# Optimization experiments

Measured on AMD Instinct MI355X. Metric: run time of the kernel, lower is better.

## Reference

```python
import jax, jax.numpy as jnp
import numpy as np

N = 100000
E = 1600000


def graph_conv(x, src, dst, W_rel, b_rel, W_root, n_nodes):
    # PyG GraphConv (aggr='add'): out = lin_rel(sum_j x_j) + lin_root(x)
    agg = jax.ops.segment_sum(x[src], dst, num_segments=n_nodes)  # [N, in]
    return agg @ W_rel + b_rel + x @ W_root


def _glorot(key, shape):
    fan_in = shape[0]
    return jax.random.normal(key, shape, dtype=jnp.float32) / jnp.sqrt(jnp.float32(fan_in))


def setup_inputs() -> dict:
    key = jax.random.key(0)
    ks = jax.random.split(key, 16)
    x = jax.random.normal(ks[0], (N, 48), dtype=jnp.float32)
    additional_x = jax.random.normal(ks[1], (N, 16), dtype=jnp.float32)
    lf_embedding = jax.random.normal(ks[2], (N, 16), dtype=jnp.float32)
    edge_index = jax.random.randint(ks[3], (2, E), 0, N, dtype=jnp.int64)
    # conv1: 64 -> 32 ; conv2: 48 -> 48 ; conv3: 48 -> 16
    return {
        "x": x,
        "edge_index": edge_index,
        "additional_x": additional_x,
        "lf_embedding": lf_embedding,
        "W1_rel": _glorot(ks[4], (64, 32)),
        "b1": jnp.zeros((32,), dtype=jnp.float32),
        "W1_root": _glorot(ks[5], (64, 32)),
        "W2_rel": _glorot(ks[6], (48, 48)),
        "b2": jnp.zeros((48,), dtype=jnp.float32),
        "W2_root": _glorot(ks[7], (48, 48)),
        "W3_rel": _glorot(ks[8], (48, 16)),
        "b3": jnp.zeros((16,), dtype=jnp.float32),
        "W3_root": _glorot(ks[9], (48, 16)),
    }


def reference(x, edge_index, additional_x, lf_embedding,
              W1_rel, b1, W1_root, W2_rel, b2, W2_root, W3_rel, b3, W3_root):
    src, dst = edge_index[0], edge_index[1]
    n = x.shape[0]
    h = jnp.concatenate([x, additional_x], axis=1)            # [N, 64]
    h = jax.nn.relu(graph_conv(h, src, dst, W1_rel, b1, W1_root, n))  # [N, 32]
    h = jnp.concatenate([h, lf_embedding], axis=1)            # [N, 48]
    h = jax.nn.relu(graph_conv(h, src, dst, W2_rel, b2, W2_root, n))  # [N, 48]
    h = graph_conv(h, src, dst, W3_rel, b3, W3_root, n)       # [N, 16]
    return h + additional_x
```

## Files before the change

kernel.cpp:

```cpp
#include <hip/hip_runtime.h>

#define NODES_MAX 100000
#define EDGES_MAX 1600000
#define BN 256
#define NBUCK ((NODES_MAX + BN - 1) / BN)
#define B_PART 256
#define SCAN_CHUNK 1024

__device__ float g_ws[(size_t)NODES_MAX * 160];
__device__ unsigned short g_tb[(size_t)NODES_MAX * 112];
__device__ int g_rowptr[NODES_MAX + 1];
__device__ int g_csr[EDGES_MAX];
__device__ unsigned g_be[EDGES_MAX];
__device__ int g_mat[NBUCK * B_PART];
__device__ int g_bsum[(NBUCK * B_PART + SCAN_CHUNK - 1) / SCAN_CHUNK + 1];

__device__ __forceinline__ unsigned short f2bf(float f) {
    union { float f; unsigned u; } c; c.f = f;
    unsigned r = (c.u + 0x7FFFu + ((c.u >> 16) & 1u)) >> 16;
    return (unsigned short)r;
}
__device__ __forceinline__ float bflo(unsigned u) {
    union { unsigned u; float f; } c; c.u = u << 16; return c.f;
}
__device__ __forceinline__ float bfhi(unsigned u) {
    union { unsigned u; float f; } c; c.u = u & 0xFFFF0000u; return c.f;
}

__global__ __launch_bounds__(1024) void k_bcount(const int* __restrict__ edge, int E,
                                                 int nbuck, int chunk) {
    __shared__ int h[NBUCK];
    for (int i = threadIdx.x; i < nbuck; i += 1024) h[i] = 0;
    __syncthreads();
    const int lo = blockIdx.x * chunk, hi = min(E, lo + chunk);
    for (int e = lo + threadIdx.x; e < hi; e += 1024)
        atomicAdd(&h[edge[E + e] >> 8], 1);
    __syncthreads();
    for (int k = threadIdx.x; k < nbuck; k += 1024)
        g_mat[k * B_PART + blockIdx.x] = h[k];
}

__global__ __launch_bounds__(256) void k_scan_local(int M) {
    __shared__ int ssum[256];
    const int tid = threadIdx.x;
    const int base = blockIdx.x * SCAN_CHUNK + tid * 4;
    int v0 = (base + 0 < M) ? g_mat[base + 0] : 0;
    int v1 = (base + 1 < M) ? g_mat[base + 1] : 0;
    int v2 = (base + 2 < M) ? g_mat[base + 2] : 0;
    int v3 = (base + 3 < M) ? g_mat[base + 3] : 0;
    int s = v0 + v1 + v2 + v3;
    ssum[tid] = s;
    __syncthreads();
    for (int off = 1; off < 256; off <<= 1) {
        int v = (tid >= off) ? ssum[tid - off] : 0;
        __syncthreads();
        ssum[tid] += v;
        __syncthreads();
    }
    int run = ssum[tid] - s;
    if (base + 0 < M) g_mat[base + 0] = run;
    run += v0;
    if (base + 1 < M) g_mat[base + 1] = run;
    run += v1;
    if (base + 2 < M) g_mat[base + 2] = run;
    run += v2;
    if (base + 3 < M) g_mat[base + 3] = run;
    if (tid == 255) g_bsum[blockIdx.x] = ssum[255];
}

__global__ __launch_bounds__(1024) void k_scan_bsums(int nb) {
    __shared__ int ssum[1024];
    const int tid = threadIdx.x;
    int s = (tid < nb) ? g_bsum[tid] : 0;
    ssum[tid] = s;
    __syncthreads();
    for (int off = 1; off < 1024; off <<= 1) {
        int v = (tid >= off) ? ssum[tid - off] : 0;
        __syncthreads();
        ssum[tid] += v;
        __syncthreads();
    }
    if (tid < nb) g_bsum[tid] = ssum[tid] - s;
}

__global__ __launch_bounds__(1024) void k_bpart(const int* __restrict__ edge, int E,
                                                int nbuck, int chunk) {
    __shared__ int cur[NBUCK];
    for (int k = threadIdx.x; k < nbuck; k += 1024) {
        int idx = k * B_PART + blockIdx.x;
        cur[k] = g_mat[idx] + g_bsum[idx >> 10];
    }
    __syncthreads();
    const int lo = blockIdx.x * chunk, hi = min(E, lo + chunk);
    for (int e = lo + threadIdx.x; e < hi; e += 1024) {
        int s = edge[e], d = edge[E + e];
        int pos = atomicAdd(&cur[d >> 8], 1);
        g_be[pos] = ((unsigned)s << 8) | (unsigned)(d & (BN - 1));
    }
}

__global__ __launch_bounds__(BN) void k_csr(int N, int E, int nbuck) {
    const int b = blockIdx.x;
    const int nlo = b * BN;
    const int ebase = g_mat[b * B_PART] + g_bsum[(b * B_PART) >> 10];
    const int eend = (b + 1 < nbuck)
        ? (g_mat[(b + 1) * B_PART] + g_bsum[((b + 1) * B_PART) >> 10]) : E;
    __shared__ int cnt[BN];
    __shared__ int pfx[BN];
    const int tid = threadIdx.x;
    cnt[tid] = 0;
    __syncthreads();
    for (int e = ebase + tid; e < eend; e += BN)
        atomicAdd(&cnt[g_be[e] & (BN - 1)], 1);
    __syncthreads();
    int v = cnt[tid];
    pfx[tid] = v;
    __syncthreads();
    for (int off = 1; off < BN; off <<= 1) {
        int t = (tid >= off) ? pfx[tid - off] : 0;
        __syncthreads();
        pfx[tid] += t;
        __syncthreads();
    }
    int excl = pfx[tid] - v;
    int n = nlo + tid;
    if (n < N) g_rowptr[n] = ebase + excl;
    if (b == 0 && tid == 0) g_rowptr[N] = E;
    cnt[tid] = excl;
    __syncthreads();
    for (int e = ebase + tid; e < eend; e += BN) {
        unsigned pv = g_be[e];
        int pos = atomicAdd(&cnt[pv & (BN - 1)], 1);
        g_csr[ebase + pos] = (int)(pv >> 8);
    }
}

template <int F, int RS>
__global__ __launch_bounds__(256) void k_gather_relu(size_t oTB, size_t oR, size_t oH, int N) {
    constexpr int L = F / 8;
    int tid = blockIdx.x * 256 + threadIdx.x;
    int node = tid / L, c = tid % L;
    if (node >= N) return;
    const unsigned short* __restrict__ tb = &g_tb[oTB];
    int j = g_rowptr[node];
    const int end = g_rowptr[node + 1];
    float s0 = 0.f, s1 = 0.f, s2 = 0.f, s3 = 0.f, s4 = 0.f, s5 = 0.f, s6 = 0.f, s7 = 0.f;
    for (; j + 3 < end; j += 4) {
        int sn0 = g_csr[j], sn1 = g_csr[j + 1], sn2 = g_csr[j + 2], sn3 = g_csr[j + 3];
        const uint4 v0 = *(const uint4*)&tb[(size_t)sn0 * RS + c * 8];
        const uint4 v1 = *(const uint4*)&tb[(size_t)sn1 * RS + c * 8];
        const uint4 v2 = *(const uint4*)&tb[(size_t)sn2 * RS + c * 8];
        const uint4 v3 = *(const uint4*)&tb[(size_t)sn3 * RS + c * 8];
        s0 += bflo(v0.x) + bflo(v1.x) + bflo(v2.x) + bflo(v3.x);
        s1 += bfhi(v0.x) + bfhi(v1.x) + bfhi(v2.x) + bfhi(v3.x);
        s2 += bflo(v0.y) + bflo(v1.y) + bflo(v2.y) + bflo(v3.y);
        s3 += bfhi(v0.y) + bfhi(v1.y) + bfhi(v2.y) + bfhi(v3.y);
        s4 += bflo(v0.z) + bflo(v1.z) + bflo(v2.z) + bflo(v3.z);
        s5 += bfhi(v0.z) + bfhi(v1.z) + bfhi(v2.z) + bfhi(v3.z);
        s6 += bflo(v0.w) + bflo(v1.w) + bflo(v2.w) + bflo(v3.w);
        s7 += bfhi(v0.w) + bfhi(v1.w) + bfhi(v2.w) + bfhi(v3.w);
    }
    for (; j < end; ++j) {
        int sn = g_csr[j];
        const uint4 v = *(const uint4*)&tb[(size_t)sn * RS + c * 8];
        s0 += bflo(v.x); s1 += bfhi(v.x);
        s2 += bflo(v.y); s3 += bfhi(v.y);
        s4 += bflo(v.z); s5 += bfhi(v.z);
        s6 += bflo(v.w); s7 += bfhi(v.w);
    }
    const size_t ro = oR + (size_t)node * F + c * 8;
    const float4 ra = *(const float4*)&g_ws[ro];
    const float4 rb = *(const float4*)&g_ws[ro + 4];
    float4 oa, ob;
    oa.x = fmaxf(s0 + ra.x, 0.f); oa.y = fmaxf(s1 + ra.y, 0.f);
    oa.z = fmaxf(s2 + ra.z, 0.f); oa.w = fmaxf(s3 + ra.w, 0.f);
    ob.x = fmaxf(s4 + rb.x, 0.f); ob.y = fmaxf(s5 + rb.y, 0.f);
    ob.z = fmaxf(s6 + rb.z, 0.f); ob.w = fmaxf(s7 + rb.w, 0.f);
    const size_t ho = oH + (size_t)node * F + c * 8;
    *(float4*)&g_ws[ho] = oa;
    *(float4*)&g_ws[ho + 4] = ob;
}

__global__ __launch_bounds__(256) void k_gather_out(size_t oTB, float* __restrict__ out, int N) {
    constexpr int F = 16, L = 2;
    int tid = blockIdx.x * 256 + threadIdx.x;
    int node = tid / L, c = tid % L;
    if (node >= N) return;
    const unsigned short* __restrict__ tb = &g_tb[oTB];
    int j = g_rowptr[node];
    const int end = g_rowptr[node + 1];
    float s0 = 0.f, s1 = 0.f, s2 = 0.f, s3 = 0.f, s4 = 0.f, s5 = 0.f, s6 = 0.f, s7 = 0.f;
    for (; j + 3 < end; j += 4) {
        int sn0 = g_csr[j], sn1 = g_csr[j + 1], sn2 = g_csr[j + 2], sn3 = g_csr[j + 3];
        const uint4 v0 = *(const uint4*)&tb[(size_t)sn0 * F + c * 8];
        const uint4 v1 = *(const uint4*)&tb[(size_t)sn1 * F + c * 8];
        const uint4 v2 = *(const uint4*)&tb[(size_t)sn2 * F + c * 8];
        const uint4 v3 = *(const uint4*)&tb[(size_t)sn3 * F + c * 8];
        s0 += bflo(v0.x) + bflo(v1.x) + bflo(v2.x) + bflo(v3.x);
        s1 += bfhi(v0.x) + bfhi(v1.x) + bfhi(v2.x) + bfhi(v3.x);
        s2 += bflo(v0.y) + bflo(v1.y) + bflo(v2.y) + bflo(v3.y);
        s3 += bfhi(v0.y) + bfhi(v1.y) + bfhi(v2.y) + bfhi(v3.y);
        s4 += bflo(v0.z) + bflo(v1.z) + bflo(v2.z) + bflo(v3.z);
        s5 += bfhi(v0.z) + bfhi(v1.z) + bfhi(v2.z) + bfhi(v3.z);
        s6 += bflo(v0.w) + bflo(v1.w) + bflo(v2.w) + bflo(v3.w);
        s7 += bfhi(v0.w) + bfhi(v1.w) + bfhi(v2.w) + bfhi(v3.w);
    }
    for (; j < end; ++j) {
        int sn = g_csr[j];
        const uint4 v = *(const uint4*)&tb[(size_t)sn * F + c * 8];
        s0 += bflo(v.x); s1 += bfhi(v.x);
        s2 += bflo(v.y); s3 += bfhi(v.y);
        s4 += bflo(v.z); s5 += bfhi(v.z);
        s6 += bflo(v.w); s7 += bfhi(v.w);
    }
    float* op = &out[(size_t)node * F + c * 8];
    float4 oa = *(float4*)op;
    float4 ob = *(float4*)(op + 4);
    oa.x += s0; oa.y += s1; oa.z += s2; oa.w += s3;
    ob.x += s4; ob.y += s5; ob.z += s6; ob.w += s7;
    *(float4*)op = oa;
    *(float4*)(op + 4) = ob;
}

#define L1_PADS 72
__global__ __launch_bounds__(512) void k_l1_transform(
        const float* __restrict__ x, const float* __restrict__ ax,
        const float* __restrict__ Wrel, const float* __restrict__ Wroot,
        const float* __restrict__ b, int N, size_t oTB1, size_t oR1) {
    __shared__ float sWrel[64 * 32];
    __shared__ float sWroot[64 * 32];
    __shared__ unsigned short sH[128 * L1_PADS];
    const int tid = threadIdx.x;
    if (tid < 512) {
        ((float4*)sWrel)[tid] = ((const float4*)Wrel)[tid];
        ((float4*)sWroot)[tid] = ((const float4*)Wroot)[tid];
    }
    const int n0 = blockIdx.x * 128;
    for (int i = tid; i < 128 * 16; i += 512) {
        int nl = i >> 4, g = i & 15, n = n0 + nl;
        float4 v = {0.f, 0.f, 0.f, 0.f};
        if (n < N) v = (g < 12) ? *(const float4*)&x[(size_t)n * 48 + g * 4]
                                : *(const float4*)&ax[(size_t)n * 16 + (g - 12) * 4];
        ushort4 hv;
        hv.x = f2bf(v.x); hv.y = f2bf(v.y); hv.z = f2bf(v.z); hv.w = f2bf(v.w);
        *(ushort4*)&sH[nl * L1_PADS + g * 4] = hv;
    }
    __syncthreads();
    const int jg = tid & 7, nlp = tid >> 3;
    const unsigned short* h0p = &sH[(nlp * 2 + 0) * L1_PADS];
    const unsigned short* h1p = &sH[(nlp * 2 + 1) * L1_PADS];
    float at[2][4] = {}, ar[2][4] = {};
    for (int k = 0; k < 64; ++k) {
        const float4 wr = *(const float4*)&sWrel[k * 32 + jg * 4];
        const float4 wo = *(const float4*)&sWroot[k * 32 + jg * 4];
        const float h0 = bflo(h0p[k]);
        const float h1 = bflo(h1p[k]);
        at[0][0] = fmaf(h0, wr.x, at[0][0]); at[0][1] = fmaf(h0, wr.y, at[0][1]);
        at[0][2] = fmaf(h0, wr.z, at[0][2]); at[0][3] = fmaf(h0, wr.w, at[0][3]);
        ar[0][0] = fmaf(h0, wo.x, ar[0][0]); ar[0][1] = fmaf(h0, wo.y, ar[0][1]);
        ar[0][2] = fmaf(h0, wo.z, ar[0][2]); ar[0][3] = fmaf(h0, wo.w, ar[0][3]);
        at[1][0] = fmaf(h1, wr.x, at[1][0]); at[1][1] = fmaf(h1, wr.y, at[1][1]);
        at[1][2] = fmaf(h1, wr.z, at[1][2]); at[1][3] = fmaf(h1, wr.w, at[1][3]);
        ar[1][0] = fmaf(h1, wo.x, ar[1][0]); ar[1][1] = fmaf(h1, wo.y, ar[1][1]);
        ar[1][2] = fmaf(h1, wo.z, ar[1][2]); ar[1][3] = fmaf(h1, wo.w, ar[1][3]);
    }
    const float4 bv = *(const float4*)&b[jg * 4];
    #pragma unroll
    for (int m = 0; m < 2; ++m) {
        int n = n0 + nlp * 2 + m;
        if (n < N) {
            ushort4 tv;
            tv.x = f2bf(at[m][0]); tv.y = f2bf(at[m][1]);
            tv.z = f2bf(at[m][2]); tv.w = f2bf(at[m][3]);
            *(ushort4*)&g_tb[oTB1 + (size_t)n * 32 + jg * 4] = tv;
            float4 rv;
            rv.x = ar[m][0] + bv.x; rv.y = ar[m][1] + bv.y;
            rv.z = ar[m][2] + bv.z; rv.w = ar[m][3] + bv.w;
            *(float4*)&g_ws[oR1 + (size_t)n * 32 + jg * 4] = rv;
        }
    }
}

#define L2_PAD 49
__global__ __launch_bounds__(384) void k_l2_transform(
        const float* __restrict__ lf,
        const float* __restrict__ Wrel, const float* __restrict__ Wroot,
        const float* __restrict__ b, int N,
        size_t oH1, size_t oTB2, size_t oR2) {
    __shared__ float sWrel[48 * 48];
    __shared__ float sWroot[48 * 48];
    __shared__ float sH[64 * L2_PAD];
    const int tid = threadIdx.x;
    for (int i = tid; i < 576; i += 384) {
        ((float4*)sWrel)[i] = ((const float4*)Wrel)[i];
        ((float4*)sWroot)[i] = ((const float4*)Wroot)[i];
    }
    const int n0 = blockIdx.x * 64;
    for (int i = tid; i < 64 * 48; i += 384) {
        int nl = i / 48, k = i % 48, n = n0 + nl;
        float v = 0.f;
        if (n < N) v = (k < 32) ? g_ws[oH1 + (size_t)n * 32 + k]
                                : lf[(size_t)n * 16 + (k - 32)];
        sH[nl * L2_PAD + k] = v;
    }
    __syncthreads();
    const int jg = tid % 12, nlp = tid / 12;
    const float* h0p = &sH[(nlp * 2 + 0) * L2_PAD];
    const float* h1p = &sH[(nlp * 2 + 1) * L2_PAD];
    float at[2][4] = {}, ar[2][4] = {};
    for (int k = 0; k < 48; ++k) {
        const float4 wr = *(const float4*)&sWrel[k * 48 + jg * 4];
        const float4 wo = *(const float4*)&sWroot[k * 48 + jg * 4];
        const float h0 = h0p[k];
        const float h1 = h1p[k];
        at[0][0] = fmaf(h0, wr.x, at[0][0]); at[0][1] = fmaf(h0, wr.y, at[0][1]);
        at[0][2] = fmaf(h0, wr.z, at[0][2]); at[0][3] = fmaf(h0, wr.w, at[0][3]);
        ar[0][0] = fmaf(h0, wo.x, ar[0][0]); ar[0][1] = fmaf(h0, wo.y, ar[0][1]);
        ar[0][2] = fmaf(h0, wo.z, ar[0][2]); ar[0][3] = fmaf(h0, wo.w, ar[0][3]);
        at[1][0] = fmaf(h1, wr.x, at[1][0]); at[1][1] = fmaf(h1, wr.y, at[1][1]);
        at[1][2] = fmaf(h1, wr.z, at[1][2]); at[1][3] = fmaf(h1, wr.w, at[1][3]);
        ar[1][0] = fmaf(h1, wo.x, ar[1][0]); ar[1][1] = fmaf(h1, wo.y, ar[1][1]);
        ar[1][2] = fmaf(h1, wo.z, ar[1][2]); ar[1][3] = fmaf(h1, wo.w, ar[1][3]);
    }
    const float4 bv = *(const float4*)&b[jg * 4];
    #pragma unroll
    for (int m = 0; m < 2; ++m) {
        int n = n0 + nlp * 2 + m;
        if (n < N) {
            ushort4 tv;
            tv.x = f2bf(at[m][0]); tv.y = f2bf(at[m][1]);
            tv.z = f2bf(at[m][2]); tv.w = f2bf(at[m][3]);
            *(ushort4*)&g_tb[oTB2 + (size_t)n * 64 + jg * 4] = tv;
            float4 rv;
            rv.x = ar[m][0] + bv.x; rv.y = ar[m][1] + bv.y;
            rv.z = ar[m][2] + bv.z; rv.w = ar[m][3] + bv.w;
            *(float4*)&g_ws[oR2 + (size_t)n * 48 + jg * 4] = rv;
        }
    }
}

#define L3_PAD 49
__global__ __launch_bounds__(256) void k_l3_transform(
        const float* __restrict__ ax,
        const float* __restrict__ Wrel, const float* __restrict__ Wroot,
        const float* __restrict__ b, int N,
        size_t oH2, size_t oTB3, float* __restrict__ out) {
    __shared__ float sWrel[48 * 16];
    __shared__ float sWroot[48 * 16];
    __shared__ float sH[128 * L3_PAD];
    const int tid = threadIdx.x;
    if (tid < 192) {
        ((float4*)sWrel)[tid] = ((const float4*)Wrel)[tid];
        ((float4*)sWroot)[tid] = ((const float4*)Wroot)[tid];
    }
    const int n0 = blockIdx.x * 128;
    for (int i = tid; i < 128 * 48; i += 256) {
        int nl = i / 48, k = i % 48, n = n0 + nl;
        sH[nl * L3_PAD + k] = (n < N) ? g_ws[oH2 + (size_t)n * 48 + k] : 0.f;
    }
    __syncthreads();
    const int jg = tid & 3, nlp = tid >> 2;
    const float* h0p = &sH[(nlp * 2 + 0) * L3_PAD];
    const float* h1p = &sH[(nlp * 2 + 1) * L3_PAD];
    float at[2][4] = {}, ar[2][4] = {};
    for (int k = 0; k < 48; ++k) {
        const float4 wr = *(const float4*)&sWrel[k * 16 + jg * 4];
        const float4 wo = *(const float4*)&sWroot[k * 16 + jg * 4];
        const float h0 = h0p[k];
        const float h1 = h1p[k];
        at[0][0] = fmaf(h0, wr.x, at[0][0]); at[0][1] = fmaf(h0, wr.y, at[0][1]);
        at[0][2] = fmaf(h0, wr.z, at[0][2]); at[0][3] = fmaf(h0, wr.w, at[0][3]);
        ar[0][0] = fmaf(h0, wo.x, ar[0][0]); ar[0][1] = fmaf(h0, wo.y, ar[0][1]);
        ar[0][2] = fmaf(h0, wo.z, ar[0][2]); ar[0][3] = fmaf(h0, wo.w, ar[0][3]);
        at[1][0] = fmaf(h1, wr.x, at[1][0]); at[1][1] = fmaf(h1, wr.y, at[1][1]);
        at[1][2] = fmaf(h1, wr.z, at[1][2]); at[1][3] = fmaf(h1, wr.w, at[1][3]);
        ar[1][0] = fmaf(h1, wo.x, ar[1][0]); ar[1][1] = fmaf(h1, wo.y, ar[1][1]);
        ar[1][2] = fmaf(h1, wo.z, ar[1][2]); ar[1][3] = fmaf(h1, wo.w, ar[1][3]);
    }
    const float4 bv = *(const float4*)&b[jg * 4];
    #pragma unroll
    for (int m = 0; m < 2; ++m) {
        int n = n0 + nlp * 2 + m;
        if (n < N) {
            ushort4 tv;
            tv.x = f2bf(at[m][0]); tv.y = f2bf(at[m][1]);
            tv.z = f2bf(at[m][2]); tv.w = f2bf(at[m][3]);
            *(ushort4*)&g_tb[oTB3 + (size_t)n * 16 + jg * 4] = tv;
            const float4 av = *(const float4*)&ax[(size_t)n * 16 + jg * 4];
            float4 rv;
            rv.x = ar[m][0] + bv.x + av.x; rv.y = ar[m][1] + bv.y + av.y;
            rv.z = ar[m][2] + bv.z + av.z; rv.w = ar[m][3] + bv.w + av.w;
            *(float4*)&out[(size_t)n * 16 + jg * 4] = rv;
        }
    }
}

extern "C" void kernel_launch(void* const* d_in, const int* in_sizes, int n_in,
                              void* d_out, int out_size, void* d_ws, size_t ws_size,
                              hipStream_t stream) {
    const float* x     = (const float*)d_in[0];
    const int*   edge  = (const int*)d_in[1];
    const float* ax    = (const float*)d_in[2];
    const float* lf    = (const float*)d_in[3];
    const float* W1rel = (const float*)d_in[4];
    const float* b1    = (const float*)d_in[5];
    const float* W1root= (const float*)d_in[6];
    const float* W2rel = (const float*)d_in[7];
    const float* b2    = (const float*)d_in[8];
    const float* W2root= (const float*)d_in[9];
    const float* W3rel = (const float*)d_in[10];
    const float* b3    = (const float*)d_in[11];
    const float* W3root= (const float*)d_in[12];
    float* out = (float*)d_out;

    const int N = in_sizes[0] / 48;
    const int E = in_sizes[1] / 2;
    const int nbuck = (N + BN - 1) / BN;
    const int chunk = (E + B_PART - 1) / B_PART;
    const int M = nbuck * B_PART;
    const int nb = (M + SCAN_CHUNK - 1) / SCAN_CHUNK;

    const size_t oR1 = 0;
    const size_t oH1 = (size_t)N * 32;
    const size_t oR2 = (size_t)N * 64;
    const size_t oH2 = (size_t)N * 112;
    const size_t oTB1 = 0;
    const size_t oTB2 = (size_t)N * 32;
    const size_t oTB3 = (size_t)N * 96;

    k_bcount<<<B_PART, 1024, 0, stream>>>(edge, E, nbuck, chunk);
    k_scan_local<<<nb, 256, 0, stream>>>(M);
    k_scan_bsums<<<1, 1024, 0, stream>>>(nb);
    k_bpart<<<B_PART, 1024, 0, stream>>>(edge, E, nbuck, chunk);
    k_csr<<<nbuck, BN, 0, stream>>>(N, E, nbuck);

    k_l1_transform<<<(N + 127) / 128, 512, 0, stream>>>(x, ax, W1rel, W1root, b1, N, oTB1, oR1);
    k_gather_relu<32, 32><<<(unsigned)(((size_t)N * 4 + 255) / 256), 256, 0, stream>>>(oTB1, oR1, oH1, N);
    k_l2_transform<<<(N + 63) / 64, 384, 0, stream>>>(lf, W2rel, W2root, b2, N, oH1, oTB2, oR2);
    k_gather_relu<48, 64><<<(unsigned)(((size_t)N * 6 + 255) / 256), 256, 0, stream>>>(oTB2, oR2, oH2, N);
    k_l3_transform<<<(N + 127) / 128, 256, 0, stream>>>(ax, W3rel, W3root, b3, N, oH2, oTB3, out);
    k_gather_out<<<(unsigned)(((size_t)N * 2 + 255) / 256), 256, 0, stream>>>(oTB3, out, N);
}
```

Baseline: 278.0 us.

## Sort nodes by in-degree to balance gather work across wavefront lanes

Adds three kernels that bin nodes by in-degree (histogram per block, scan, scatter) into a permutation, then the gather kernels process nodes in degree-sorted order. Lanes in a wavefront then get similar loop trip counts, which is meant to reduce divergence and idle lanes in the neighbour-sum loops. In exchange it adds three launches, an extra indirection per thread, and scattered writes to the h and out buffers, since consecutive threads no longer map to consecutive nodes.

```diff
diff --git a/kernel.cpp b/kernel.cpp
--- a/kernel.cpp
+++ b/kernel.cpp
@@ -6,6 +6,8 @@
 #define NBUCK ((NODES_MAX + BN - 1) / BN)
 #define B_PART 256
 #define SCAN_CHUNK 1024
+#define PB 128
+#define DBIN 64
 
 __device__ float g_ws[(size_t)NODES_MAX * 160];
 __device__ unsigned short g_tb[(size_t)NODES_MAX * 112];
@@ -14,6 +16,8 @@
 __device__ unsigned g_be[EDGES_MAX];
 __device__ int g_mat[NBUCK * B_PART];
 __device__ int g_bsum[(NBUCK * B_PART + SCAN_CHUNK - 1) / SCAN_CHUNK + 1];
+__device__ int g_dmat[DBIN * PB];
+__device__ int g_perm[NODES_MAX];
 
 __device__ __forceinline__ unsigned short f2bf(float f) {
     union { float f; unsigned u; } c; c.f = f;
@@ -135,12 +139,58 @@
     }
 }
 
+__global__ __launch_bounds__(256) void k_dcount(int N, int chunk) {
+    __shared__ int h[DBIN];
+    if (threadIdx.x < DBIN) h[threadIdx.x] = 0;
+    __syncthreads();
+    const int lo = blockIdx.x * chunk, hi = min(N, lo + chunk);
+    for (int n = lo + threadIdx.x; n < hi; n += 256) {
+        int deg = min(g_rowptr[n + 1] - g_rowptr[n], DBIN - 1);
+        atomicAdd(&h[deg], 1);
+    }
+    __syncthreads();
+    if (threadIdx.x < DBIN) g_dmat[threadIdx.x * PB + blockIdx.x] = h[threadIdx.x];
+}
+
+__global__ __launch_bounds__(1024) void k_dscan() {
+    __shared__ int ssum[1024];
+    const int tid = threadIdx.x;
+    const int base = tid * 8;
+    int v[8]; int s = 0;
+    #pragma unroll
+    for (int i = 0; i < 8; ++i) { v[i] = g_dmat[base + i]; s += v[i]; }
+    ssum[tid] = s;
+    __syncthreads();
+    for (int off = 1; off < 1024; off <<= 1) {
+        int t = (tid >= off) ? ssum[tid - off] : 0;
+        __syncthreads();
+        ssum[tid] += t;
+        __syncthreads();
+    }
+    int run = ssum[tid] - s;
+    #pragma unroll
+    for (int i = 0; i < 8; ++i) { int d = v[i]; g_dmat[base + i] = run; run += d; }
+}
+
+__global__ __launch_bounds__(256) void k_dperm(int N, int chunk) {
+    __shared__ int cur[DBIN];
+    if (threadIdx.x < DBIN) cur[threadIdx.x] = g_dmat[threadIdx.x * PB + blockIdx.x];
+    __syncthreads();
+    const int lo = blockIdx.x * chunk, hi = min(N, lo + chunk);
+    for (int n = lo + threadIdx.x; n < hi; n += 256) {
+        int deg = min(g_rowptr[n + 1] - g_rowptr[n], DBIN - 1);
+        int pos = atomicAdd(&cur[deg], 1);
+        g_perm[pos] = n;
+    }
+}
+
 template <int F, int RS>
 __global__ __launch_bounds__(256) void k_gather_relu(size_t oTB, size_t oR, size_t oH, int N) {
     constexpr int L = F / 8;
     int tid = blockIdx.x * 256 + threadIdx.x;
-    int node = tid / L, c = tid % L;
-    if (node >= N) return;
+    int gid = tid / L, c = tid % L;
+    if (gid >= N) return;
+    const int node = g_perm[gid];
     const unsigned short* __restrict__ tb = &g_tb[oTB];
     int j = g_rowptr[node];
     const int end = g_rowptr[node + 1];
@@ -184,8 +234,9 @@
 __global__ __launch_bounds__(256) void k_gather_out(size_t oTB, float* __restrict__ out, int N) {
     constexpr int F = 16, L = 2;
     int tid = blockIdx.x * 256 + threadIdx.x;
-    int node = tid / L, c = tid % L;
-    if (node >= N) return;
+    int gid = tid / L, c = tid % L;
+    if (gid >= N) return;
+    const int node = g_perm[gid];
     const unsigned short* __restrict__ tb = &g_tb[oTB];
     int j = g_rowptr[node];
     const int end = g_rowptr[node + 1];
@@ -419,6 +470,7 @@
     const int chunk = (E + B_PART - 1) / B_PART;
     const int M = nbuck * B_PART;
     const int nb = (M + SCAN_CHUNK - 1) / SCAN_CHUNK;
+    const int pchunk = (N + PB - 1) / PB;
 
     const size_t oR1 = 0;
     const size_t oH1 = (size_t)N * 32;
@@ -433,6 +485,9 @@
     k_scan_bsums<<<1, 1024, 0, stream>>>(nb);
     k_bpart<<<B_PART, 1024, 0, stream>>>(edge, E, nbuck, chunk);
     k_csr<<<nbuck, BN, 0, stream>>>(N, E, nbuck);
+    k_dcount<<<PB, 256, 0, stream>>>(N, pchunk);
+    k_dscan<<<1, 1024, 0, stream>>>();
+    k_dperm<<<PB, 256, 0, stream>>>(N, pchunk);
 
     k_l1_transform<<<(N + 127) / 128, 512, 0, stream>>>(x, ax, W1rel, W1root, b1, N, oTB1, oR1);
     k_gather_relu<32, 32><<<(unsigned)(((size_t)N * 4 + 255) / 256), 256, 0, stream>>>(oTB1, oR1, oH1, N);
```

Measured after the change: 335.5 us. 1.21x slower.
